# Kernel optimization log

Measured on AMD Instinct MI355X. Metric: run time of the kernel, lower is better.

## Reference

```python
import jax, jax.numpy as jnp
import numpy as np

D_MODEL = 19
N_HEADS = 8
D_HEAD = 64
SCALE = float(np.sqrt(512.0 / 9.0))  # module hardcodes sqrt(512/9)


def setup_inputs() -> dict:
    key = jax.random.key(0)
    ks = jax.random.split(key, 12)
    B, L = 16, 1024
    H = N_HEADS * D_HEAD  # 512
    s_in = 1.0 / np.sqrt(D_MODEL)
    s_out = 1.0 / np.sqrt(H)
    return {
        "Q": jax.random.normal(ks[0], (B, L, D_MODEL), jnp.float32),
        "K": jax.random.normal(ks[1], (B, L, D_MODEL), jnp.float32),
        "V": jax.random.normal(ks[2], (B, L, D_MODEL), jnp.float32),
        "attn_mask": jax.random.randint(ks[3], (B, L, L), 0, 2).astype(bool),
        "Wq": jax.random.normal(ks[4], (D_MODEL, H), jnp.float32) * s_in,
        "bq": jnp.zeros((H,), jnp.float32),
        "Wk": jax.random.normal(ks[5], (D_MODEL, H), jnp.float32) * s_in,
        "bk": jnp.zeros((H,), jnp.float32),
        "Wv": jax.random.normal(ks[6], (D_MODEL, H), jnp.float32) * s_in,
        "bv": jnp.zeros((H,), jnp.float32),
        "Wo": jax.random.normal(ks[7], (H, D_MODEL), jnp.float32) * s_out,
        "bo": jnp.zeros((D_MODEL,), jnp.float32),
        "ln_g": jnp.ones((D_MODEL,), jnp.float32),
        "ln_b": jnp.zeros((D_MODEL,), jnp.float32),
    }


def _layer_norm(x, g, b, eps=1e-5):
    mu = jnp.mean(x, axis=-1, keepdims=True)
    var = jnp.var(x, axis=-1, keepdims=True)
    return (x - mu) * jax.lax.rsqrt(var + eps) * g + b


def reference(Q, K, V, attn_mask, Wq, bq, Wk, bk, Wv, bv, Wo, bo, ln_g, ln_b):
    B, Lq, _ = Q.shape
    residual = Q
    # projections -> [B, H, L, d]
    q = (Q @ Wq + bq).reshape(B, Lq, N_HEADS, D_HEAD).transpose(0, 2, 1, 3)
    k = (K @ Wk + bk).reshape(B, -1, N_HEADS, D_HEAD).transpose(0, 2, 1, 3)
    v = (V @ Wv + bv).reshape(B, -1, N_HEADS, D_HEAD).transpose(0, 2, 1, 3)
    # scores [B, H, Lq, Lk]
    scores = jnp.einsum("bhqd,bhkd->bhqk", q, k) / SCALE
    scores = jnp.where(attn_mask[:, None, :, :], -1e9, scores)
    attn = jax.nn.softmax(scores, axis=-1)
    context = jnp.einsum("bhqk,bhkd->bhqd", attn, v)
    context = context.transpose(0, 2, 1, 3).reshape(B, Lq, N_HEADS * D_HEAD)
    output = context @ Wo + bo
    out = _layer_norm(output + residual, ln_g, ln_b)
    return (out, attn, residual)
```

## Files before the change

kernel.cpp:

```cpp
#include <hip/hip_runtime.h>
#include <hip/hip_bf16.h>
#include <stdint.h>


#define LQ 1024
#define DM 19
#define NHEAD 8
#define DH 64
#define HT 512
#define NBATCH 16

using f32x4  = __attribute__((ext_vector_type(4))) float;
using bf16x8 = __attribute__((ext_vector_type(8))) __bf16;
using ushort_t = unsigned short;

#define INV_SCALE 0.13258252147247766f

__device__ __forceinline__ ushort_t f2bf(float f) {
  union { float f; unsigned u; } v; v.f = f;
  unsigned r = v.u + 0x7FFFu + ((v.u >> 16) & 1u);
  return (ushort_t)(r >> 16);
}

__global__ void k_prep(const unsigned char* __restrict__ m, int* __restrict__ flag,
                       const float* __restrict__ Wo, ushort_t* __restrict__ wobT) {
  if (blockIdx.x == 0) {
    __shared__ int any;
    if (threadIdx.x == 0) any = 0;
    __syncthreads();
    int loc = 0;
    for (int i = threadIdx.x; i < 16384; i += 256)
      if (i & 3) loc |= m[i];
    if (loc) any = 1;
    __syncthreads();
    if (threadIdx.x == 0) *flag = (any != 0);
  }
  const int i = blockIdx.x * 256 + threadIdx.x;
  const int j = i >> 9, k = i & 511;
  wobT[i] = (j < DM) ? f2bf(Wo[k * DM + j]) : (ushort_t)0;
}

__global__ __launch_bounds__(256, 4) void k_proj(
    const float* __restrict__ Q, const float* __restrict__ K, const float* __restrict__ V,
    const float* __restrict__ Wq, const float* __restrict__ bq,
    const float* __restrict__ Wk, const float* __restrict__ bk,
    const float* __restrict__ Wv, const float* __restrict__ bv,
    ushort_t* __restrict__ qb, ushort_t* __restrict__ kb, ushort_t* __restrict__ vT) {
  const int bid = blockIdx.x;
  const int bh = bid >> 4;
  const int lt = (bid & 15) * 64;
  const int b  = bh >> 3;
  const int h  = bh & 7;
  const int t  = threadIdx.x;

  __shared__ float xs[3][64 * DM];
  __shared__ ushort_t vt[64 * 73];

  const int rowbase = (b * LQ + lt) * DM;
  for (int i = t; i < 64 * DM; i += 256) {
    xs[0][i] = Q[rowbase + i];
    xs[1][i] = K[rowbase + i];
    xs[2][i] = V[rowbase + i];
  }
  __syncthreads();

  const int d = t & 63;
  const int w = t >> 6;

  float wq[DM], wk[DM], wv[DM];
#pragma unroll
  for (int j = 0; j < DM; ++j) {
    wq[j] = Wq[j * HT + h * DH + d];
    wk[j] = Wk[j * HT + h * DH + d];
    wv[j] = Wv[j * HT + h * DH + d];
  }
  const float bqv = bq[h * DH + d], bkv = bk[h * DH + d], bvv = bv[h * DH + d];
  const size_t outb = ((size_t)bh * LQ + lt) * DH;

  for (int it = 0; it < 16; ++it) {
    const int r = it * 4 + w;
    float aq = bqv, ak = bkv, av = bvv;
#pragma unroll
    for (int j = 0; j < DM; ++j) {
      const float xq = xs[0][r * DM + j], xk = xs[1][r * DM + j], xv = xs[2][r * DM + j];
      aq += xq * wq[j];
      ak += xk * wk[j];
      av += xv * wv[j];
    }
    qb[outb + (size_t)r * DH + d] = f2bf(aq);
    kb[outb + (size_t)r * DH + d] = f2bf(ak);
    vt[r * 73 + d] = f2bf(av);
  }
  __syncthreads();

  const size_t vbase = (size_t)bh * DH * LQ + lt;
  for (int it = 0; it < 16; ++it) {
    const int e = t + 256 * it;
    const int dd = e >> 6, rr = e & 63;
    vT[vbase + (size_t)dd * LQ + rr] = vt[rr * 73 + dd];
  }
}

__global__ __launch_bounds__(256) void k_attn2(
    const ushort_t* __restrict__ qb, const ushort_t* __restrict__ kb,
    const ushort_t* __restrict__ vT, const void* __restrict__ maskp,
    const int* __restrict__ flagp,
    float* __restrict__ attn, ushort_t* __restrict__ ctxb) {
  const int bid = blockIdx.x;
  const int swz = (bid & 7) * 256 + (bid >> 3);
  const int t = threadIdx.x;
  const int w = t >> 6, lane = t & 63;
  const int qtile = swz * 4 + w;
  const int bh = qtile >> 6, qt = qtile & 63;
  const int bidx = bh >> 3, h = bh & 7;
  const int q0 = qt * 16;
  const int g = lane >> 4, c = lane & 15;

  __shared__ float ps[4][16 * 36];

  const int msh = (*flagp) ? 0 : 2;
  const unsigned char* mB = (const unsigned char*)maskp;

  const ushort_t* qrow = qb + ((size_t)(bh * LQ + q0 + c)) * DH + 8 * g;
  const bf16x8 aq0 = *(const bf16x8*)(qrow);
  const bf16x8 aq1 = *(const bf16x8*)(qrow + 32);

  size_t mrow[4];
#pragma unroll
  for (int r = 0; r < 4; ++r)
    mrow[r] = ((size_t)(bidx * LQ + q0 + 4 * g + r)) * LQ;

  float sum[4] = {0.f, 0.f, 0.f, 0.f};
#pragma unroll 4
  for (int kt = 0; kt < 64; ++kt) {
    const ushort_t* krow = kb + ((size_t)(bh * LQ + kt * 16 + c)) * DH + 8 * g;
    const bf16x8 b0 = *(const bf16x8*)(krow);
    const bf16x8 b1 = *(const bf16x8*)(krow + 32);
    f32x4 s4 = (f32x4){0.f, 0.f, 0.f, 0.f};
    s4 = __builtin_amdgcn_mfma_f32_16x16x32_bf16(aq0, b0, s4, 0, 0, 0);
    s4 = __builtin_amdgcn_mfma_f32_16x16x32_bf16(aq1, b1, s4, 0, 0, 0);
    const int col = kt * 16 + c;
#pragma unroll
    for (int r = 0; r < 4; ++r) {
      const unsigned char mv = mB[(mrow[r] + col) << msh];
      const float p = __expf(s4[r] * INV_SCALE);
      sum[r] += mv ? 0.f : p;
    }
  }
#pragma unroll
  for (int r = 0; r < 4; ++r) {
    sum[r] += __shfl_xor(sum[r], 1);
    sum[r] += __shfl_xor(sum[r], 2);
    sum[r] += __shfl_xor(sum[r], 4);
    sum[r] += __shfl_xor(sum[r], 8);
  }
  float inv[4];
#pragma unroll
  for (int r = 0; r < 4; ++r) inv[r] = 1.0f / sum[r];

  float* myps = ps[w];
  f32x4 acc2[4];
#pragma unroll
  for (int cf = 0; cf < 4; ++cf) acc2[cf] = (f32x4){0.f, 0.f, 0.f, 0.f};

  const int srow = lane >> 3, sc4 = lane & 7;
  const size_t abase = ((size_t)(bh * LQ) + q0 + srow) * LQ + sc4 * 4;

  for (int ck = 0; ck < 32; ++ck) {
    const int kc = ck * 32;
    const ushort_t* kr0 = kb + ((size_t)(bh * LQ + kc + c)) * DH + 8 * g;
    const ushort_t* kr1 = kr0 + 16 * DH;
    f32x4 s0 = (f32x4){0.f, 0.f, 0.f, 0.f};
    f32x4 s1 = (f32x4){0.f, 0.f, 0.f, 0.f};
    s0 = __builtin_amdgcn_mfma_f32_16x16x32_bf16(aq0, *(const bf16x8*)(kr0), s0, 0, 0, 0);
    s0 = __builtin_amdgcn_mfma_f32_16x16x32_bf16(aq1, *(const bf16x8*)(kr0 + 32), s0, 0, 0, 0);
    s1 = __builtin_amdgcn_mfma_f32_16x16x32_bf16(aq0, *(const bf16x8*)(kr1), s1, 0, 0, 0);
    s1 = __builtin_amdgcn_mfma_f32_16x16x32_bf16(aq1, *(const bf16x8*)(kr1 + 32), s1, 0, 0, 0);
#pragma unroll
    for (int r = 0; r < 4; ++r) {
      const unsigned char m0 = mB[(mrow[r] + kc + c) << msh];
      const unsigned char m1 = mB[(mrow[r] + kc + 16 + c) << msh];
      const float p0 = m0 ? 0.f : __expf(s0[r] * INV_SCALE) * inv[r];
      const float p1 = m1 ? 0.f : __expf(s1[r] * INV_SCALE) * inv[r];
      myps[(4 * g + r) * 36 + c] = p0;
      myps[(4 * g + r) * 36 + 16 + c] = p1;
    }
    const f32x4 pa0 = *(const f32x4*)&myps[c * 36 + 8 * g];
    const f32x4 pa1 = *(const f32x4*)&myps[c * 36 + 8 * g + 4];
    bf16x8 pa;
#pragma unroll
    for (int i = 0; i < 4; ++i) {
      pa[i]     = (__bf16)pa0[i];
      pa[i + 4] = (__bf16)pa1[i];
    }
    const f32x4 v0 = *(const f32x4*)&myps[srow * 36 + sc4 * 4];
    const f32x4 v1 = *(const f32x4*)&myps[(srow + 8) * 36 + sc4 * 4];
    __builtin_nontemporal_store(v0, (f32x4*)&attn[abase + kc]);
    __builtin_nontemporal_store(v1, (f32x4*)&attn[abase + 8 * LQ + kc]);
#pragma unroll
    for (int cf = 0; cf < 4; ++cf) {
      const ushort_t* vr = vT + ((size_t)(bh * DH + cf * 16 + c)) * LQ + kc + 8 * g;
      const bf16x8 bv = *(const bf16x8*)(vr);
      acc2[cf] = __builtin_amdgcn_mfma_f32_16x16x32_bf16(pa, bv, acc2[cf], 0, 0, 0);
    }
  }

  ushort_t* cps = (ushort_t*)myps;
#pragma unroll
  for (int cf = 0; cf < 4; ++cf)
#pragma unroll
    for (int r = 0; r < 4; ++r)
      cps[(4 * g + r) * 72 + cf * 16 + c] = f2bf(acc2[cf][r]);

  const int o8 = (lane & 7) * 8;
  const f32x4 c0 = *(const f32x4*)&cps[srow * 72 + o8];
  const f32x4 c1 = *(const f32x4*)&cps[(srow + 8) * 72 + o8];
  const size_t cb = ((size_t)(bidx * LQ) + q0 + srow) * HT + h * DH + o8;
  *(f32x4*)&ctxb[cb] = c0;
  *(f32x4*)&ctxb[cb + 8 * HT] = c1;
}

__global__ __launch_bounds__(256) void k_out2(
    const ushort_t* __restrict__ ctxb, const ushort_t* __restrict__ wobT,
    const float* __restrict__ bo, const float* __restrict__ Qin,
    const float* __restrict__ lng, const float* __restrict__ lnb,
    float* __restrict__ out) {
  const int t = threadIdx.x;
  const int w = t >> 6, lane = t & 63;
  const int g = lane >> 4, c = lane & 15;
  const int grow0 = blockIdx.x * 64 + w * 16;

  f32x4 acc0 = (f32x4){0.f, 0.f, 0.f, 0.f};
  f32x4 acc1 = (f32x4){0.f, 0.f, 0.f, 0.f};
#pragma unroll
  for (int kt = 0; kt < 16; ++kt) {
    const bf16x8 a  = *(const bf16x8*)&ctxb[((size_t)(grow0 + c)) * HT + kt * 32 + 8 * g];
    const bf16x8 b0 = *(const bf16x8*)&wobT[(size_t)c * HT + kt * 32 + 8 * g];
    const bf16x8 b1 = *(const bf16x8*)&wobT[(size_t)(c + 16) * HT + kt * 32 + 8 * g];
    acc0 = __builtin_amdgcn_mfma_f32_16x16x32_bf16(a, b0, acc0, 0, 0, 0);
    acc1 = __builtin_amdgcn_mfma_f32_16x16x32_bf16(a, b1, acc1, 0, 0, 0);
  }

  const bool v1 = (c < 3);
  const float bo0 = bo[c];
  const float bo1 = v1 ? bo[16 + c] : 0.f;
  const float g0 = lng[c], b0v = lnb[c];
  const float g1 = v1 ? lng[16 + c] : 0.f;
  const float b1v = v1 ? lnb[16 + c] : 0.f;

#pragma unroll
  for (int r = 0; r < 4; ++r) {
    const int grow = grow0 + 4 * g + r;
    const float x0 = acc0[r] + bo0 + Qin[(size_t)grow * DM + c];
    const float x1 = v1 ? (acc1[r] + bo1 + Qin[(size_t)grow * DM + 16 + c]) : 0.f;
    float s = x0 + x1;
    float q = x0 * x0 + x1 * x1;
    s += __shfl_xor(s, 1);  q += __shfl_xor(q, 1);
    s += __shfl_xor(s, 2);  q += __shfl_xor(q, 2);
    s += __shfl_xor(s, 4);  q += __shfl_xor(q, 4);
    s += __shfl_xor(s, 8);  q += __shfl_xor(q, 8);
    const float mean = s * (1.0f / (float)DM);
    const float var = q * (1.0f / (float)DM) - mean * mean;
    const float rstd = rsqrtf(var + 1e-5f);
    out[(size_t)grow * DM + c] = (x0 - mean) * rstd * g0 + b0v;
    if (v1) out[(size_t)grow * DM + 16 + c] = (x1 - mean) * rstd * g1 + b1v;
  }
}

extern "C" void kernel_launch(void* const* d_in, const int* in_sizes, int n_in,
                              void* d_out, int out_size, void* d_ws, size_t ws_size,
                              hipStream_t stream) {
  const float* Q  = (const float*)d_in[0];
  const float* K  = (const float*)d_in[1];
  const float* V  = (const float*)d_in[2];
  const void*  mask = d_in[3];
  const float* Wq = (const float*)d_in[4];
  const float* bq = (const float*)d_in[5];
  const float* Wk = (const float*)d_in[6];
  const float* bk = (const float*)d_in[7];
  const float* Wv = (const float*)d_in[8];
  const float* bv = (const float*)d_in[9];
  const float* Wo = (const float*)d_in[10];
  const float* bo = (const float*)d_in[11];
  const float* lng = (const float*)d_in[12];
  const float* lnb = (const float*)d_in[13];

  float* out   = (float*)d_out;
  float* attn  = out + 311296;
  float* resid = out + 311296 + 134217728;

  ushort_t* qb   = (ushort_t*)d_ws;
  ushort_t* kb   = (ushort_t*)((char*)d_ws + 16777216);
  ushort_t* vT   = (ushort_t*)((char*)d_ws + 33554432);
  ushort_t* ctxb = (ushort_t*)((char*)d_ws + 50331648);
  ushort_t* wobT = (ushort_t*)((char*)d_ws + 67108864);
  int* flag      = (int*)((char*)d_ws + 67108864 + 32768);

  hipMemcpyAsync(resid, Q, (size_t)311296 * sizeof(float),
                 hipMemcpyDeviceToDevice, stream);

  k_prep<<<64, 256, 0, stream>>>((const unsigned char*)mask, flag, Wo, wobT);
  k_proj<<<2048, 256, 0, stream>>>(Q, K, V, Wq, bq, Wk, bk, Wv, bv, qb, kb, vT);
  k_attn2<<<2048, 256, 0, stream>>>(qb, kb, vT, mask, flag, attn, ctxb);
  k_out2<<<256, 256, 0, stream>>>(ctxb, wobT, bo, Q, lng, lnb, out);
}
```

Baseline: 1.191 ms.

## Pack mask to bits, split keys across waves, compute scores once

A new kernel packs the boolean mask into 32-bit bitmasks, so the attention kernel reads one word per row per 32 keys instead of bytes. The attention kernel now gives one 16-query tile to four waves that each cover a quarter of the keys. Each wave keeps its exponentials in registers, so QK^T and exp are computed once rather than twice. Row sums and partial context are combined across waves through shared memory with block barriers, which adds an extra launch, more registers and synchronisation.

```diff
diff --git a/kernel.cpp b/kernel.cpp
--- a/kernel.cpp
+++ b/kernel.cpp
@@ -13,6 +13,7 @@
 using f32x4  = __attribute__((ext_vector_type(4))) float;
 using bf16x8 = __attribute__((ext_vector_type(8))) __bf16;
 using ushort_t = unsigned short;
+using uint_t = unsigned int;
 
 #define INV_SCALE 0.13258252147247766f
 
@@ -40,6 +41,33 @@
   wobT[i] = (j < DM) ? f2bf(Wo[k * DM + j]) : (ushort_t)0;
 }
 
+__global__ void k_maskpack(const void* __restrict__ maskp, const int* __restrict__ flagp,
+                           uint_t* __restrict__ bits) {
+  const int i = blockIdx.x * 256 + threadIdx.x;
+  uint_t b = 0;
+  if (*flagp) {
+    const uint4* p = (const uint4*)((const char*)maskp + 32 * (size_t)i);
+    const uint4 a = p[0], d = p[1];
+    const uint_t wv[8] = {a.x, a.y, a.z, a.w, d.x, d.y, d.z, d.w};
+#pragma unroll
+    for (int jw = 0; jw < 8; ++jw)
+#pragma unroll
+      for (int by = 0; by < 4; ++by)
+        if ((wv[jw] >> (8 * by)) & 0xFFu) b |= 1u << (jw * 4 + by);
+  } else {
+    const uint4* p = (const uint4*)((const char*)maskp + 128 * (size_t)i);
+#pragma unroll
+    for (int jw = 0; jw < 8; ++jw) {
+      const uint4 v = p[jw];
+      b |= (uint_t)(v.x != 0) << (4 * jw);
+      b |= (uint_t)(v.y != 0) << (4 * jw + 1);
+      b |= (uint_t)(v.z != 0) << (4 * jw + 2);
+      b |= (uint_t)(v.w != 0) << (4 * jw + 3);
+    }
+  }
+  bits[i] = b;
+}
+
 __global__ __launch_bounds__(256, 4) void k_proj(
     const float* __restrict__ Q, const float* __restrict__ K, const float* __restrict__ V,
     const float* __restrict__ Wq, const float* __restrict__ bq,
@@ -101,73 +129,38 @@
   }
 }
 
-__global__ __launch_bounds__(256) void k_attn2(
+__global__ __launch_bounds__(256, 4) void k_attn3(
     const ushort_t* __restrict__ qb, const ushort_t* __restrict__ kb,
-    const ushort_t* __restrict__ vT, const void* __restrict__ maskp,
-    const int* __restrict__ flagp,
+    const ushort_t* __restrict__ vT, const uint_t* __restrict__ bits,
     float* __restrict__ attn, ushort_t* __restrict__ ctxb) {
   const int bid = blockIdx.x;
-  const int swz = (bid & 7) * 256 + (bid >> 3);
-  const int t = threadIdx.x;
-  const int w = t >> 6, lane = t & 63;
-  const int qtile = swz * 4 + w;
-  const int bh = qtile >> 6, qt = qtile & 63;
+  const int qg  = (bid & 7) * 1024 + (bid >> 3);
+  const int bh  = qg >> 6, qt = qg & 63;
   const int bidx = bh >> 3, h = bh & 7;
-  const int q0 = qt * 16;
-  const int g = lane >> 4, c = lane & 15;
-
-  __shared__ float ps[4][16 * 36];
-
-  const int msh = (*flagp) ? 0 : 2;
-  const unsigned char* mB = (const unsigned char*)maskp;
+  const int q0   = qt * 16;
+  const int t    = threadIdx.x;
+  const int w    = t >> 6, lane = t & 63;
+  const int g    = lane >> 4, c = lane & 15;
+  const int k0   = w * 256;
+
+  __shared__ float ps[4][2][16 * 36];
+  __shared__ float c2s[4][16][64];
+  __shared__ float wsum[4][16];
 
   const ushort_t* qrow = qb + ((size_t)(bh * LQ + q0 + c)) * DH + 8 * g;
   const bf16x8 aq0 = *(const bf16x8*)(qrow);
   const bf16x8 aq1 = *(const bf16x8*)(qrow + 32);
 
-  size_t mrow[4];
+  const uint_t* brow[4];
 #pragma unroll
   for (int r = 0; r < 4; ++r)
-    mrow[r] = ((size_t)(bidx * LQ + q0 + 4 * g + r)) * LQ;
-
+    brow[r] = bits + ((size_t)(bidx * LQ + q0 + 4 * g + r)) * 32;
+
+  f32x4 acc[16];
   float sum[4] = {0.f, 0.f, 0.f, 0.f};
-#pragma unroll 4
-  for (int kt = 0; kt < 64; ++kt) {
-    const ushort_t* krow = kb + ((size_t)(bh * LQ + kt * 16 + c)) * DH + 8 * g;
-    const bf16x8 b0 = *(const bf16x8*)(krow);
-    const bf16x8 b1 = *(const bf16x8*)(krow + 32);
-    f32x4 s4 = (f32x4){0.f, 0.f, 0.f, 0.f};
-    s4 = __builtin_amdgcn_mfma_f32_16x16x32_bf16(aq0, b0, s4, 0, 0, 0);
-    s4 = __builtin_amdgcn_mfma_f32_16x16x32_bf16(aq1, b1, s4, 0, 0, 0);
-    const int col = kt * 16 + c;
-#pragma unroll
-    for (int r = 0; r < 4; ++r) {
-      const unsigned char mv = mB[(mrow[r] + col) << msh];
-      const float p = __expf(s4[r] * INV_SCALE);
-      sum[r] += mv ? 0.f : p;
-    }
-  }
-#pragma unroll
-  for (int r = 0; r < 4; ++r) {
-    sum[r] += __shfl_xor(sum[r], 1);
-    sum[r] += __shfl_xor(sum[r], 2);
-    sum[r] += __shfl_xor(sum[r], 4);
-    sum[r] += __shfl_xor(sum[r], 8);
-  }
-  float inv[4];
-#pragma unroll
-  for (int r = 0; r < 4; ++r) inv[r] = 1.0f / sum[r];
-
-  float* myps = ps[w];
-  f32x4 acc2[4];
-#pragma unroll
-  for (int cf = 0; cf < 4; ++cf) acc2[cf] = (f32x4){0.f, 0.f, 0.f, 0.f};
-
-  const int srow = lane >> 3, sc4 = lane & 7;
-  const size_t abase = ((size_t)(bh * LQ) + q0 + srow) * LQ + sc4 * 4;
-
-  for (int ck = 0; ck < 32; ++ck) {
-    const int kc = ck * 32;
+#pragma unroll
+  for (int j = 0; j < 8; ++j) {
+    const int kc = k0 + j * 32;
     const ushort_t* kr0 = kb + ((size_t)(bh * LQ + kc + c)) * DH + 8 * g;
     const ushort_t* kr1 = kr0 + 16 * DH;
     f32x4 s0 = (f32x4){0.f, 0.f, 0.f, 0.f};
@@ -176,14 +169,51 @@
     s0 = __builtin_amdgcn_mfma_f32_16x16x32_bf16(aq1, *(const bf16x8*)(kr0 + 32), s0, 0, 0, 0);
     s1 = __builtin_amdgcn_mfma_f32_16x16x32_bf16(aq0, *(const bf16x8*)(kr1), s1, 0, 0, 0);
     s1 = __builtin_amdgcn_mfma_f32_16x16x32_bf16(aq1, *(const bf16x8*)(kr1 + 32), s1, 0, 0, 0);
+    const int wi = kc >> 5;
 #pragma unroll
     for (int r = 0; r < 4; ++r) {
-      const unsigned char m0 = mB[(mrow[r] + kc + c) << msh];
-      const unsigned char m1 = mB[(mrow[r] + kc + 16 + c) << msh];
-      const float p0 = m0 ? 0.f : __expf(s0[r] * INV_SCALE) * inv[r];
-      const float p1 = m1 ? 0.f : __expf(s1[r] * INV_SCALE) * inv[r];
-      myps[(4 * g + r) * 36 + c] = p0;
-      myps[(4 * g + r) * 36 + 16 + c] = p1;
+      const uint_t mw = brow[r][wi];
+      const float e0 = ((mw >> c) & 1u) ? 0.f : __expf(s0[r] * INV_SCALE);
+      const float e1 = ((mw >> (16 + c)) & 1u) ? 0.f : __expf(s1[r] * INV_SCALE);
+      acc[2 * j][r] = e0;
+      acc[2 * j + 1][r] = e1;
+      sum[r] += e0 + e1;
+    }
+  }
+#pragma unroll
+  for (int r = 0; r < 4; ++r) {
+    sum[r] += __shfl_xor(sum[r], 1);
+    sum[r] += __shfl_xor(sum[r], 2);
+    sum[r] += __shfl_xor(sum[r], 4);
+    sum[r] += __shfl_xor(sum[r], 8);
+  }
+  if (c == 0) {
+#pragma unroll
+    for (int r = 0; r < 4; ++r) wsum[w][4 * g + r] = sum[r];
+  }
+  __syncthreads();
+  float inv[4];
+#pragma unroll
+  for (int r = 0; r < 4; ++r) {
+    const int rr = 4 * g + r;
+    inv[r] = 1.0f / (wsum[0][rr] + wsum[1][rr] + wsum[2][rr] + wsum[3][rr]);
+  }
+
+  f32x4 acc2[4];
+#pragma unroll
+  for (int cf = 0; cf < 4; ++cf) acc2[cf] = (f32x4){0.f, 0.f, 0.f, 0.f};
+
+  const int srow = lane >> 3, sc4 = lane & 7;
+  const size_t abase = ((size_t)(bh * LQ) + q0 + srow) * LQ + sc4 * 4;
+
+#pragma unroll
+  for (int j = 0; j < 8; ++j) {
+    const int kc = k0 + j * 32;
+    float* myps = ps[w][j & 1];
+#pragma unroll
+    for (int r = 0; r < 4; ++r) {
+      myps[(4 * g + r) * 36 + c]      = acc[2 * j][r] * inv[r];
+      myps[(4 * g + r) * 36 + 16 + c] = acc[2 * j + 1][r] * inv[r];
     }
     const f32x4 pa0 = *(const f32x4*)&myps[c * 36 + 8 * g];
     const f32x4 pa1 = *(const f32x4*)&myps[c * 36 + 8 * g + 4];
@@ -205,19 +235,20 @@
     }
   }
 
-  ushort_t* cps = (ushort_t*)myps;
 #pragma unroll
   for (int cf = 0; cf < 4; ++cf)
 #pragma unroll
     for (int r = 0; r < 4; ++r)
-      cps[(4 * g + r) * 72 + cf * 16 + c] = f2bf(acc2[cf][r]);
-
-  const int o8 = (lane & 7) * 8;
-  const f32x4 c0 = *(const f32x4*)&cps[srow * 72 + o8];
-  const f32x4 c1 = *(const f32x4*)&cps[(srow + 8) * 72 + o8];
-  const size_t cb = ((size_t)(bidx * LQ) + q0 + srow) * HT + h * DH + o8;
-  *(f32x4*)&ctxb[cb] = c0;
-  *(f32x4*)&ctxb[cb + 8 * HT] = c1;
+      c2s[w][4 * g + r][cf * 16 + c] = acc2[cf][r];
+  __syncthreads();
+
+#pragma unroll
+  for (int i0 = 0; i0 < 4; ++i0) {
+    const int i = t + i0 * 256;
+    const int r = i >> 6, d = i & 63;
+    const float s = c2s[0][r][d] + c2s[1][r][d] + c2s[2][r][d] + c2s[3][r][d];
+    ctxb[((size_t)(bidx * LQ + q0 + r)) * HT + h * DH + d] = f2bf(s);
+  }
 }
 
 __global__ __launch_bounds__(256) void k_out2(
@@ -295,12 +326,14 @@
   ushort_t* ctxb = (ushort_t*)((char*)d_ws + 50331648);
   ushort_t* wobT = (ushort_t*)((char*)d_ws + 67108864);
   int* flag      = (int*)((char*)d_ws + 67108864 + 32768);
+  uint_t* bits   = (uint_t*)((char*)d_ws + 67108864 + 65536);
 
   hipMemcpyAsync(resid, Q, (size_t)311296 * sizeof(float),
                  hipMemcpyDeviceToDevice, stream);
 
   k_prep<<<64, 256, 0, stream>>>((const unsigned char*)mask, flag, Wo, wobT);
+  k_maskpack<<<2048, 256, 0, stream>>>(mask, flag, bits);
   k_proj<<<2048, 256, 0, stream>>>(Q, K, V, Wq, bq, Wk, bk, Wv, bv, qb, kb, vT);
-  k_attn2<<<2048, 256, 0, stream>>>(qb, kb, vT, mask, flag, attn, ctxb);
+  k_attn3<<<8192, 256, 0, stream>>>(qb, kb, vT, bits, attn, ctxb);
   k_out2<<<256, 256, 0, stream>>>(ctxb, wobT, bo, Q, lng, lnb, out);
 }
```

Result: faster. 1.005 ms (-15.7%).
